# Performance work log

Hardware: AMD Instinct MI355X
Metric: run time of the kernel (lower is better)

The kernel has to match this reference:

```python
import jax, jax.numpy as jnp
import numpy as np

MASK_VALUE = 0.0  # default `mask=0` scalar in the original forward


def setup_inputs() -> dict:
    key = jax.random.key(0)
    kq, kk, kv = jax.random.split(key, 3)
    b, n, d_k, d_v = 8, 2048, 64, 64
    q = jax.random.normal(kq, (b, n, d_k), dtype=jnp.float32)
    k = jax.random.normal(kk, (b, n, d_k), dtype=jnp.float32)
    v = jax.random.normal(kv, (b, n, d_v), dtype=jnp.float32)
    return {"q": q, "k": k, "v": v}


def reference(q, k, v):
    d_k = q.shape[-1]
    temper = jnp.asarray(d_k, q.dtype) ** 0.5
    # scores: (b, n, n)
    attn = jnp.einsum('bqd,bkd->bqk', q, k) / temper
    # equality-based masking: positions whose score exactly equals the
    # scalar `mask` (default 0) are set to -inf before softmax.
    attn = jnp.where(attn == MASK_VALUE, -jnp.inf, attn)
    # NOTE: the original code calls `attn.masked_fill(look_ahead_mask==0, -inf)`
    # WITHOUT assignment, so the look-ahead mask is a no-op; we omit it faithfully.
    attn = jax.nn.softmax(attn, axis=-1)
    out = jnp.einsum('bqk,bkd->bqd', attn, v)  # (b, n, d_v)
    return out
```

## Files before the change

### kernel.cpp

```cpp
#include <hip/hip_runtime.h>
#include <hip/hip_bf16.h>

typedef __bf16 bf16_t;
typedef bf16_t bf16x2 __attribute__((ext_vector_type(2)));
typedef bf16_t bf16x8 __attribute__((ext_vector_type(8)));
typedef float  floatx4  __attribute__((ext_vector_type(4)));
typedef float  floatx16 __attribute__((ext_vector_type(16)));

constexpr int B = 8, N = 2048, D = 64;

__global__ __launch_bounds__(256)
void prepass_kernel(const float* __restrict__ k, const float* __restrict__ v,
                    bf16_t* __restrict__ kf, bf16_t* __restrict__ vf) {
    __shared__ float t[32 * 65];
    const int tid = threadIdx.x;
    const int b   = blockIdx.x & 7;
    const int kvb = blockIdx.x >> 3;
    const size_t inoff  = ((size_t)b * N + kvb * 32) * D;
    const size_t outoff = (size_t)(b * 64 + kvb) * 2048;

    {
        const float* src = k + inoff;
        floatx4 f0 = *(const floatx4*)(src + tid * 8);
        floatx4 f1 = *(const floatx4*)(src + tid * 8 + 4);
        bf16x8 o;
        #pragma unroll
        for (int j = 0; j < 4; ++j) { o[j] = (bf16_t)f0[j]; o[j + 4] = (bf16_t)f1[j]; }
        const int rr = tid >> 3, kd = (tid >> 1) & 3, hh = tid & 1;
        *(bf16x8*)(kf + outoff + (size_t)kd * 512 + (hh * 32 + rr) * 8) = o;
    }
    {
        const float* src = v + inoff;
        floatx4 f0 = *(const floatx4*)(src + tid * 8);
        floatx4 f1 = *(const floatx4*)(src + tid * 8 + 4);
        const int rr = tid >> 3, cc = (tid & 7) * 8;
        #pragma unroll
        for (int j = 0; j < 4; ++j) { t[rr * 65 + cc + j] = f0[j]; t[rr * 65 + cc + 4 + j] = f1[j]; }
        __syncthreads();
        const int s2 = tid >> 7, dblk = (tid >> 6) & 1, lane = tid & 63;
        const int hh = lane >> 5, l31 = lane & 31;
        bf16x8 o;
        #pragma unroll
        for (int j = 0; j < 8; ++j)
            o[j] = (bf16_t)t[(s2 * 16 + hh * 8 + j) * 65 + dblk * 32 + l31];
        *(bf16x8*)(vf + outoff + (size_t)(s2 * 2 + dblk) * 512 + lane * 8) = o;
    }
}

__global__ __launch_bounds__(512, 4)
void attn_kernel(const float* __restrict__ q, const bf16_t* __restrict__ kf,
                 const bf16_t* __restrict__ vf, float* __restrict__ out) {
    __shared__ char smem[58240];
    float* o_buf = (float*)smem;
    float* l_buf = (float*)(smem + 57344);

    const int tid  = threadIdx.x;
    const int lane = tid & 63;
    const int cg   = tid >> 6;
    const int h    = lane >> 5;
    const int l31  = lane & 31;

    const int b  = blockIdx.x & 7;
    const int q0 = (blockIdx.x >> 3) * 32;

    const bf16_t* kfb = kf + (size_t)b * 131072;
    const bf16_t* vfb = vf + (size_t)b * 131072;

    bf16x8 qf[4];
    {
        const float* qp = q + ((size_t)b * N + q0 + l31) * D + h * 8;
        #pragma unroll
        for (int kd = 0; kd < 4; ++kd) {
            floatx4 f0 = *(const floatx4*)(qp + kd * 16);
            floatx4 f1 = *(const floatx4*)(qp + kd * 16 + 4);
            bf16x8 t;
            #pragma unroll
            for (int j = 0; j < 4; ++j) {
                t[j]     = (bf16_t)(f0[j] * 0.125f);
                t[j + 4] = (bf16_t)(f1[j] * 0.125f);
            }
            qf[kd] = t;
        }
    }

    floatx16 o_acc[2];
    #pragma unroll
    for (int d = 0; d < 2; ++d)
        #pragma unroll
        for (int i = 0; i < 16; ++i) o_acc[d][i] = 0.f;
    float l_run = 0.f;

    bf16x8 kreg[4];
    #pragma unroll
    for (int kd = 0; kd < 4; ++kd)
        kreg[kd] = *(const bf16x8*)(kfb + (size_t)cg * 2048 + kd * 512 + lane * 8);

    #pragma unroll 2
    for (int it = 0; it < 8; ++it) {
        const size_t base = (size_t)(it * 8 + cg) * 2048;

        bf16x8 vreg[4];
        #pragma unroll
        for (int u = 0; u < 4; ++u)
            vreg[u] = *(const bf16x8*)(vfb + base + (size_t)u * 512 + lane * 8);

        floatx16 s;
        #pragma unroll
        for (int i = 0; i < 16; ++i) s[i] = 0.f;
        #pragma unroll
        for (int kd = 0; kd < 4; ++kd)
            s = __builtin_amdgcn_mfma_f32_32x32x16_bf16(kreg[kd], qf[kd], s, 0, 0, 0);

        if (it + 1 < 8) {
            const size_t nbase = (size_t)((it + 1) * 8 + cg) * 2048;
            #pragma unroll
            for (int kd = 0; kd < 4; ++kd)
                kreg[kd] = *(const bf16x8*)(kfb + nbase + (size_t)kd * 512 + lane * 8);
        }

        int q8[8];
        #pragma unroll
        for (int g = 0; g < 8; ++g) {
            union { int i; bf16x2 h2; } u;
            #pragma unroll
            for (int j = 0; j < 2; ++j) {
                float x = s[2 * g + j];
                float p = (x == 0.0f) ? 0.0f : __expf(x);
                l_run += p;
                u.h2[j] = (bf16_t)p;
            }
            q8[g] = u.i;
        }

        #pragma unroll
        for (int s2 = 0; s2 < 2; ++s2) {
            int r0 = __shfl_xor(q8[4 * s2 + 0], 32);
            int r1 = __shfl_xor(q8[4 * s2 + 1], 32);
            int r2 = __shfl_xor(q8[4 * s2 + 2], 32);
            int r3 = __shfl_xor(q8[4 * s2 + 3], 32);
            union { int i4[4]; bf16x8 v; } bf;
            bf.i4[0] = h ? r2 : q8[4 * s2 + 0];
            bf.i4[1] = h ? r3 : q8[4 * s2 + 1];
            bf.i4[2] = h ? q8[4 * s2 + 2] : r0;
            bf.i4[3] = h ? q8[4 * s2 + 3] : r1;
            #pragma unroll
            for (int dblk = 0; dblk < 2; ++dblk)
                o_acc[dblk] = __builtin_amdgcn_mfma_f32_32x32x16_bf16(vreg[s2 * 2 + dblk], bf.v,
                                                                      o_acc[dblk], 0, 0, 0);
        }
    }

    l_run += __shfl_xor(l_run, 32);

    if (cg > 0) {
        float* ob = o_buf + (size_t)(cg - 1) * 2048;
        #pragma unroll
        for (int dblk = 0; dblk < 2; ++dblk)
            #pragma unroll
            for (int i = 0; i < 16; ++i) {
                const int d = (i & 3) + 8 * (i >> 2) + 4 * h + dblk * 32;
                ob[d * 32 + l31] = o_acc[dblk][i];
            }
        if (h == 0) l_buf[(cg - 1) * 32 + l31] = l_run;
    }
    __syncthreads();
    if (cg == 0) {
        float lsum = l_run;
        #pragma unroll
        for (int gg = 0; gg < 7; ++gg) lsum += l_buf[gg * 32 + l31];
        const float inv_l = 1.0f / lsum;
        float* op = out + ((size_t)b * N + q0 + l31) * D;
        #pragma unroll
        for (int dblk = 0; dblk < 2; ++dblk)
            #pragma unroll
            for (int g = 0; g < 4; ++g) {
                const int d0 = 8 * g + 4 * h + dblk * 32;
                floatx4 o4;
                #pragma unroll
                for (int j = 0; j < 4; ++j) {
                    float sum = o_acc[dblk][4 * g + j];
                    #pragma unroll
                    for (int gg = 0; gg < 7; ++gg)
                        sum += o_buf[(size_t)gg * 2048 + (d0 + j) * 32 + l31];
                    o4[j] = sum * inv_l;
                }
                *(floatx4*)(op + d0) = o4;
            }
    }
}

extern "C" void kernel_launch(void* const* d_in, const int* in_sizes, int n_in,
                              void* d_out, int out_size, void* d_ws, size_t ws_size,
                              hipStream_t stream) {
    const float* q = (const float*)d_in[0];
    const float* k = (const float*)d_in[1];
    const float* v = (const float*)d_in[2];
    float* out = (float*)d_out;
    bf16_t* kfrag = (bf16_t*)d_ws;
    bf16_t* vfrag = (bf16_t*)((char*)d_ws + (size_t)B * N * D * 2);

    hipLaunchKernelGGL(prepass_kernel, dim3(512), dim3(256), 0, stream, k, v, kfrag, vfrag);
    hipLaunchKernelGGL(attn_kernel, dim3(512), dim3(512), 0, stream, q, kfrag, vfrag, out);
}
```

Baseline: 82.75 us.

## Process two 32-row query tiles per block to reuse K/V loads

```diff
diff --git a/kernel.cpp b/kernel.cpp
--- a/kernel.cpp
+++ b/kernel.cpp
@@ -47,7 +47,7 @@
     }
 }
 
-__global__ __launch_bounds__(512, 4)
+__global__ __launch_bounds__(512, 2)
 void attn_kernel(const float* __restrict__ q, const bf16_t* __restrict__ kf,
                  const bf16_t* __restrict__ vf, float* __restrict__ out) {
     __shared__ char smem[58240];
@@ -61,14 +61,15 @@
     const int l31  = lane & 31;
 
     const int b  = blockIdx.x & 7;
-    const int q0 = (blockIdx.x >> 3) * 32;
+    const int q0 = (blockIdx.x >> 3) * 64;
 
     const bf16_t* kfb = kf + (size_t)b * 131072;
     const bf16_t* vfb = vf + (size_t)b * 131072;
 
-    bf16x8 qf[4];
-    {
-        const float* qp = q + ((size_t)b * N + q0 + l31) * D + h * 8;
+    bf16x8 qf[2][4];
+    #pragma unroll
+    for (int tqt = 0; tqt < 2; ++tqt) {
+        const float* qp = q + ((size_t)b * N + q0 + tqt * 32 + l31) * D + h * 8;
         #pragma unroll
         for (int kd = 0; kd < 4; ++kd) {
             floatx4 f0 = *(const floatx4*)(qp + kd * 16);
@@ -79,23 +80,25 @@
                 t[j]     = (bf16_t)(f0[j] * 0.125f);
                 t[j + 4] = (bf16_t)(f1[j] * 0.125f);
             }
-            qf[kd] = t;
-        }
-    }
-
-    floatx16 o_acc[2];
+            qf[tqt][kd] = t;
+        }
+    }
+
+    floatx16 o_acc[2][2];
     #pragma unroll
-    for (int d = 0; d < 2; ++d)
-        #pragma unroll
-        for (int i = 0; i < 16; ++i) o_acc[d][i] = 0.f;
-    float l_run = 0.f;
+    for (int tqt = 0; tqt < 2; ++tqt)
+        #pragma unroll
+        for (int d = 0; d < 2; ++d)
+            #pragma unroll
+            for (int i = 0; i < 16; ++i) o_acc[tqt][d][i] = 0.f;
+    float l_run[2] = {0.f, 0.f};
 
     bf16x8 kreg[4];
     #pragma unroll
     for (int kd = 0; kd < 4; ++kd)
         kreg[kd] = *(const bf16x8*)(kfb + (size_t)cg * 2048 + kd * 512 + lane * 8);
 
-    #pragma unroll 2
+    #pragma unroll 1
     for (int it = 0; it < 8; ++it) {
         const size_t base = (size_t)(it * 8 + cg) * 2048;
 
@@ -104,12 +107,14 @@
         for (int u = 0; u < 4; ++u)
             vreg[u] = *(const bf16x8*)(vfb + base + (size_t)u * 512 + lane * 8);
 
-        floatx16 s;
-        #pragma unroll
-        for (int i = 0; i < 16; ++i) s[i] = 0.f;
-        #pragma unroll
-        for (int kd = 0; kd < 4; ++kd)
-            s = __builtin_amdgcn_mfma_f32_32x32x16_bf16(kreg[kd], qf[kd], s, 0, 0, 0);
+        floatx16 sa, sb;
+        #pragma unroll
+        for (int i = 0; i < 16; ++i) { sa[i] = 0.f; sb[i] = 0.f; }
+        #pragma unroll
+        for (int kd = 0; kd < 4; ++kd) {
+            sa = __builtin_amdgcn_mfma_f32_32x32x16_bf16(kreg[kd], qf[0][kd], sa, 0, 0, 0);
+            sb = __builtin_amdgcn_mfma_f32_32x32x16_bf16(kreg[kd], qf[1][kd], sb, 0, 0, 0);
+        }
 
         if (it + 1 < 8) {
             const size_t nbase = (size_t)((it + 1) * 8 + cg) * 2048;
@@ -118,74 +123,82 @@
                 kreg[kd] = *(const bf16x8*)(kfb + nbase + (size_t)kd * 512 + lane * 8);
         }
 
-        int q8[8];
-        #pragma unroll
-        for (int g = 0; g < 8; ++g) {
-            union { int i; bf16x2 h2; } u;
-            #pragma unroll
-            for (int j = 0; j < 2; ++j) {
-                float x = s[2 * g + j];
-                float p = (x == 0.0f) ? 0.0f : __expf(x);
-                l_run += p;
-                u.h2[j] = (bf16_t)p;
+        #pragma unroll
+        for (int tqt = 0; tqt < 2; ++tqt) {
+            const floatx16& s = tqt ? sb : sa;
+            int q8[8];
+            #pragma unroll
+            for (int g = 0; g < 8; ++g) {
+                union { int i; bf16x2 h2; } u;
+                #pragma unroll
+                for (int j = 0; j < 2; ++j) {
+                    float x = s[2 * g + j];
+                    float p = (x == 0.0f) ? 0.0f : __expf(x);
+                    l_run[tqt] += p;
+                    u.h2[j] = (bf16_t)p;
+                }
+                q8[g] = u.i;
             }
-            q8[g] = u.i;
-        }
-
-        #pragma unroll
-        for (int s2 = 0; s2 < 2; ++s2) {
-            int r0 = __shfl_xor(q8[4 * s2 + 0], 32);
-            int r1 = __shfl_xor(q8[4 * s2 + 1], 32);
-            int r2 = __shfl_xor(q8[4 * s2 + 2], 32);
-            int r3 = __shfl_xor(q8[4 * s2 + 3], 32);
-            union { int i4[4]; bf16x8 v; } bf;
-            bf.i4[0] = h ? r2 : q8[4 * s2 + 0];
-            bf.i4[1] = h ? r3 : q8[4 * s2 + 1];
-            bf.i4[2] = h ? q8[4 * s2 + 2] : r0;
-            bf.i4[3] = h ? q8[4 * s2 + 3] : r1;
+            #pragma unroll
+            for (int s2 = 0; s2 < 2; ++s2) {
+                int r0 = __shfl_xor(q8[4 * s2 + 0], 32);
+                int r1 = __shfl_xor(q8[4 * s2 + 1], 32);
+                int r2 = __shfl_xor(q8[4 * s2 + 2], 32);
+                int r3 = __shfl_xor(q8[4 * s2 + 3], 32);
+                union { int i4[4]; bf16x8 v; } bf;
+                bf.i4[0] = h ? r2 : q8[4 * s2 + 0];
+                bf.i4[1] = h ? r3 : q8[4 * s2 + 1];
+                bf.i4[2] = h ? q8[4 * s2 + 2] : r0;
+                bf.i4[3] = h ? q8[4 * s2 + 3] : r1;
+                #pragma unroll
+                for (int dblk = 0; dblk < 2; ++dblk)
+                    o_acc[tqt][dblk] = __builtin_amdgcn_mfma_f32_32x32x16_bf16(
+                        vreg[s2 * 2 + dblk], bf.v, o_acc[tqt][dblk], 0, 0, 0);
+            }
+        }
+    }
+
+    l_run[0] += __shfl_xor(l_run[0], 32);
+    l_run[1] += __shfl_xor(l_run[1], 32);
+
+    #pragma unroll 1
+    for (int tqt = 0; tqt < 2; ++tqt) {
+        if (tqt) __syncthreads();
+        if (cg > 0) {
+            float* ob = o_buf + (size_t)(cg - 1) * 2048;
             #pragma unroll
             for (int dblk = 0; dblk < 2; ++dblk)
-                o_acc[dblk] = __builtin_amdgcn_mfma_f32_32x32x16_bf16(vreg[s2 * 2 + dblk], bf.v,
-                                                                      o_acc[dblk], 0, 0, 0);
-        }
-    }
-
-    l_run += __shfl_xor(l_run, 32);
-
-    if (cg > 0) {
-        float* ob = o_buf + (size_t)(cg - 1) * 2048;
-        #pragma unroll
-        for (int dblk = 0; dblk < 2; ++dblk)
-            #pragma unroll
-            for (int i = 0; i < 16; ++i) {
-                const int d = (i & 3) + 8 * (i >> 2) + 4 * h + dblk * 32;
-                ob[d * 32 + l31] = o_acc[dblk][i];
-            }
-        if (h == 0) l_buf[(cg - 1) * 32 + l31] = l_run;
-    }
-    __syncthreads();
-    if (cg == 0) {
-        float lsum = l_run;
-        #pragma unroll
-        for (int gg = 0; gg < 7; ++gg) lsum += l_buf[gg * 32 + l31];
-        const float inv_l = 1.0f / lsum;
-        float* op = out + ((size_t)b * N + q0 + l31) * D;
-        #pragma unroll
-        for (int dblk = 0; dblk < 2; ++dblk)
-            #pragma unroll
-            for (int g = 0; g < 4; ++g) {
-                const int d0 = 8 * g + 4 * h + dblk * 32;
-                floatx4 o4;
-                #pragma unroll
-                for (int j = 0; j < 4; ++j) {
-                    float sum = o_acc[dblk][4 * g + j];
+                #pragma unroll
+                for (int i = 0; i < 16; ++i) {
+                    const int d = (i & 3) + 8 * (i >> 2) + 4 * h + dblk * 32;
+                    ob[d * 32 + l31] = o_acc[tqt][dblk][i];
+                }
+            if (h == 0) l_buf[(cg - 1) * 32 + l31] = l_run[tqt];
+        }
+        __syncthreads();
+        if (cg == 0) {
+            float lsum = l_run[tqt];
+            #pragma unroll
+            for (int gg = 0; gg < 7; ++gg) lsum += l_buf[gg * 32 + l31];
+            const float inv_l = 1.0f / lsum;
+            float* op = out + ((size_t)b * N + q0 + tqt * 32 + l31) * D;
+            #pragma unroll
+            for (int dblk = 0; dblk < 2; ++dblk)
+                #pragma unroll
+                for (int g = 0; g < 4; ++g) {
+                    const int d0 = 8 * g + 4 * h + dblk * 32;
+                    floatx4 o4;
                     #pragma unroll
-                    for (int gg = 0; gg < 7; ++gg)
-                        sum += o_buf[(size_t)gg * 2048 + (d0 + j) * 32 + l31];
-                    o4[j] = sum * inv_l;
+                    for (int j = 0; j < 4; ++j) {
+                        float sum = o_acc[tqt][dblk][4 * g + j];
+                        #pragma unroll
+                        for (int gg = 0; gg < 7; ++gg)
+                            sum += o_buf[(size_t)gg * 2048 + (d0 + j) * 32 + l31];
+                        o4[j] = sum * inv_l;
+                    }
+                    *(floatx4*)(op + d0) = o4;
                 }
-                *(floatx4*)(op + d0) = o4;
-            }
+        }
     }
 }
 
@@ -200,5 +213,5 @@
     bf16_t* vfrag = (bf16_t*)((char*)d_ws + (size_t)B * N * D * 2);
 
     hipLaunchKernelGGL(prepass_kernel, dim3(512), dim3(256), 0, stream, k, v, kfrag, vfrag);
-    hipLaunchKernelGGL(attn_kernel, dim3(512), dim3(512), 0, stream, q, kfrag, vfrag, out);
+    hipLaunchKernelGGL(attn_kernel, dim3(256), dim3(512), 0, stream, q, kfrag, vfrag, out);
 }
```

Result: slower. 119.5 us (+44.5%).
